# Kernel tuning notes

Measured on AMD Instinct MI355X. Metric: run time of the kernel, lower is better.

Reference implementation:

```python
import jax, jax.numpy as jnp
import numpy as np

ALPHA = 0.65
R = 0.5

def setup_inputs() -> dict:
    key = jax.random.key(0)
    k1, k2 = jax.random.split(key)
    B, L = 8192, 2048
    output = jax.random.normal(k1, (B, L, 2), dtype=jnp.float32)
    labels = jax.random.randint(k2, (B, L), 0, 2, dtype=jnp.int64)
    return {"output": output, "labels": labels}

def reference(output, labels):
    # r[i,j] = [(1-alpha)/r, 0] if label==1 else [0, alpha/(1-r)]
    pos = jnp.asarray([(1.0 - ALPHA) / R, 0.0], dtype=output.dtype)      # label == 1
    neg = jnp.asarray([0.0, ALPHA / (1.0 - R)], dtype=output.dtype)      # label != 1
    mask = (labels == 1)[..., None]                                      # [B, L, 1]
    r = jnp.where(mask, pos, neg)                                        # [B, L, 2]
    return jnp.sum(output * r) / output.shape[0]
```

## Files before the change

kernel.cpp:

```cpp
#include <hip/hip_runtime.h>


#define BICUT_BLOCKS 2048
#define BICUT_THREADS 256

typedef float f32x4 __attribute__((ext_vector_type(4)));
typedef int   i32x2 __attribute__((ext_vector_type(2)));

__global__ __launch_bounds__(BICUT_THREADS) void bicut_partial_kernel(
    const float* __restrict__ outp,
    const int*   __restrict__ labs,
    float* __restrict__ partials,
    int n_f4,
    int n_pairs)
{
    const float CPOS = 0.7f;
    const float CNEG = 1.3f;

    const f32x4* out4 = (const f32x4*)outp;
    const i32x2* lab2 = (const i32x2*)labs;

    float acc = 0.0f;
    int stride = gridDim.x * blockDim.x;
    int tid = blockIdx.x * blockDim.x + threadIdx.x;
    #pragma unroll 4
    for (int i = tid; i < n_f4; i += stride) {
        f32x4 a = __builtin_nontemporal_load(&out4[i]);
        i32x2 l = __builtin_nontemporal_load(&lab2[i]);
        acc += (l.x == 1) ? CPOS * a.x : CNEG * a.y;
        acc += (l.y == 1) ? CPOS * a.z : CNEG * a.w;
    }
    for (int i = 2 * n_f4 + tid; i < n_pairs; i += stride) {
        acc += (labs[i] == 1) ? CPOS * outp[2 * i] : CNEG * outp[2 * i + 1];
    }

    #pragma unroll
    for (int off = 32; off > 0; off >>= 1)
        acc += __shfl_down(acc, off, 64);

    __shared__ float lds[BICUT_THREADS / 64];
    int lane = threadIdx.x & 63;
    int wave = threadIdx.x >> 6;
    if (lane == 0) lds[wave] = acc;
    __syncthreads();
    if (threadIdx.x == 0) {
        float s = 0.0f;
        #pragma unroll
        for (int w = 0; w < BICUT_THREADS / 64; ++w) s += lds[w];
        partials[blockIdx.x] = s;
    }
}

__global__ __launch_bounds__(BICUT_THREADS) void bicut_final_kernel(
    const float* __restrict__ partials,
    float* __restrict__ out,
    int n,
    float inv_b)
{
    float acc = 0.0f;
    for (int i = threadIdx.x; i < n; i += BICUT_THREADS) acc += partials[i];

    #pragma unroll
    for (int off = 32; off > 0; off >>= 1)
        acc += __shfl_down(acc, off, 64);

    __shared__ float lds[BICUT_THREADS / 64];
    int lane = threadIdx.x & 63;
    int wave = threadIdx.x >> 6;
    if (lane == 0) lds[wave] = acc;
    __syncthreads();
    if (threadIdx.x == 0) {
        float s = 0.0f;
        #pragma unroll
        for (int w = 0; w < BICUT_THREADS / 64; ++w) s += lds[w];
        out[0] = s * inv_b;
    }
}

extern "C" void kernel_launch(void* const* d_in, const int* in_sizes, int n_in,
                              void* d_out, int out_size, void* d_ws, size_t ws_size,
                              hipStream_t stream) {
    const float* output = (const float*)d_in[0];
    const int*   labels = (const int*)d_in[1];
    float* out = (float*)d_out;
    float* partials = (float*)d_ws;

    int n_pairs = in_sizes[1];
    int n_f4 = n_pairs / 2;
    const float inv_b = 1.0f / 8192.0f;

    bicut_partial_kernel<<<BICUT_BLOCKS, BICUT_THREADS, 0, stream>>>(
        output, labels, partials, n_f4, n_pairs);
    bicut_final_kernel<<<1, BICUT_THREADS, 0, stream>>>(
        partials, out, BICUT_BLOCKS, inv_b);
}
```

Measured before the change: 218.9 us.

## Fuse final reduction into partial kernel via last-block atomic ticket

```diff
diff --git a/kernel.cpp b/kernel.cpp
--- a/kernel.cpp
+++ b/kernel.cpp
@@ -7,12 +7,15 @@
 typedef float f32x4 __attribute__((ext_vector_type(4)));
 typedef int   i32x2 __attribute__((ext_vector_type(2)));
 
-__global__ __launch_bounds__(BICUT_THREADS) void bicut_partial_kernel(
+__global__ __launch_bounds__(BICUT_THREADS) void bicut_fused_kernel(
     const float* __restrict__ outp,
     const int*   __restrict__ labs,
     float* __restrict__ partials,
+    unsigned int* __restrict__ ticket,
+    float* __restrict__ out,
     int n_f4,
-    int n_pairs)
+    int n_pairs,
+    float inv_b)
 {
     const float CPOS = 0.7f;
     const float CNEG = 1.3f;
@@ -23,7 +26,7 @@
     float acc = 0.0f;
     int stride = gridDim.x * blockDim.x;
     int tid = blockIdx.x * blockDim.x + threadIdx.x;
-    #pragma unroll 4
+    #pragma unroll 8
     for (int i = tid; i < n_f4; i += stride) {
         f32x4 a = __builtin_nontemporal_load(&out4[i]);
         i32x2 l = __builtin_nontemporal_load(&lab2[i]);
@@ -39,6 +42,7 @@
         acc += __shfl_down(acc, off, 64);
 
     __shared__ float lds[BICUT_THREADS / 64];
+    __shared__ bool last;
     int lane = threadIdx.x & 63;
     int wave = threadIdx.x >> 6;
     if (lane == 0) lds[wave] = acc;
@@ -47,33 +51,33 @@
         float s = 0.0f;
         #pragma unroll
         for (int w = 0; w < BICUT_THREADS / 64; ++w) s += lds[w];
-        partials[blockIdx.x] = s;
+        __hip_atomic_store(&partials[blockIdx.x], s, __ATOMIC_RELAXED,
+                           __HIP_MEMORY_SCOPE_AGENT);
+        __threadfence();
+        unsigned int v = __hip_atomic_fetch_add(ticket, 1u, __ATOMIC_ACQ_REL,
+                                                __HIP_MEMORY_SCOPE_AGENT);
+        last = (v == gridDim.x - 1);
     }
-}
+    __syncthreads();
 
-__global__ __launch_bounds__(BICUT_THREADS) void bicut_final_kernel(
-    const float* __restrict__ partials,
-    float* __restrict__ out,
-    int n,
-    float inv_b)
-{
-    float acc = 0.0f;
-    for (int i = threadIdx.x; i < n; i += BICUT_THREADS) acc += partials[i];
-
-    #pragma unroll
-    for (int off = 32; off > 0; off >>= 1)
-        acc += __shfl_down(acc, off, 64);
-
-    __shared__ float lds[BICUT_THREADS / 64];
-    int lane = threadIdx.x & 63;
-    int wave = threadIdx.x >> 6;
-    if (lane == 0) lds[wave] = acc;
-    __syncthreads();
-    if (threadIdx.x == 0) {
-        float s = 0.0f;
+    if (last) {
+        __threadfence();
+        float a2 = 0.0f;
+        int nb = gridDim.x;
+        for (int i = threadIdx.x; i < nb; i += BICUT_THREADS)
+            a2 += __hip_atomic_load(&partials[i], __ATOMIC_RELAXED,
+                                    __HIP_MEMORY_SCOPE_AGENT);
         #pragma unroll
-        for (int w = 0; w < BICUT_THREADS / 64; ++w) s += lds[w];
-        out[0] = s * inv_b;
+        for (int off = 32; off > 0; off >>= 1)
+            a2 += __shfl_down(a2, off, 64);
+        if (lane == 0) lds[wave] = a2;
+        __syncthreads();
+        if (threadIdx.x == 0) {
+            float s = 0.0f;
+            #pragma unroll
+            for (int w = 0; w < BICUT_THREADS / 64; ++w) s += lds[w];
+            out[0] = s * inv_b;
+        }
     }
 }
 
@@ -84,13 +88,13 @@
     const int*   labels = (const int*)d_in[1];
     float* out = (float*)d_out;
     float* partials = (float*)d_ws;
+    unsigned int* ticket = (unsigned int*)(partials + BICUT_BLOCKS);
 
     int n_pairs = in_sizes[1];
     int n_f4 = n_pairs / 2;
     const float inv_b = 1.0f / 8192.0f;
 
-    bicut_partial_kernel<<<BICUT_BLOCKS, BICUT_THREADS, 0, stream>>>(
-        output, labels, partials, n_f4, n_pairs);
-    bicut_final_kernel<<<1, BICUT_THREADS, 0, stream>>>(
-        partials, out, BICUT_BLOCKS, inv_b);
+    hipMemsetAsync(ticket, 0, sizeof(unsigned int), stream);
+    bicut_fused_kernel<<<BICUT_BLOCKS, BICUT_THREADS, 0, stream>>>(
+        output, labels, partials, ticket, out, n_f4, n_pairs, inv_b);
 }
```

Result: slower. 406.1 us (+85.5%).
